# Performance work log

Hardware: AMD Instinct MI355X
Metric: run time of the kernel (lower is better)

Reference implementation:

```python
import jax, jax.numpy as jnp
import numpy as np

S_GRID = 7
B_BOX = 2
N_CLS = 20
N_CH = B_BOX * 5 + N_CLS  # 30
LAMBDA_OBJ = 5.0
LAMBDA_NOOBJ = 0.5
CI = np.array([4, 9])
BI = np.array([0, 1, 2, 3, 5, 6, 7, 8])


def setup_inputs() -> dict:
    key = jax.random.key(0)
    k1, k2 = jax.random.split(key)
    batch = 512
    P = jax.random.uniform(k1, (batch, S_GRID, S_GRID, N_CH), dtype=jnp.float32)
    T = jax.random.uniform(k2, (batch, S_GRID, S_GRID, N_CH), dtype=jnp.float32)
    # deterministic object mask: 1/8 of cells are 'object' cells (channel 4 == 1 exactly)
    cell_idx = jnp.arange(batch * S_GRID * S_GRID).reshape(batch, S_GRID, S_GRID)
    obj_mask = (cell_idx % 8 == 0).astype(jnp.float32)
    T = T.at[..., 4].set(obj_mask)
    return {"P": P, "T": T}


def _norm2dnorm(b, S):
    # (cx, cy, w, h) -> (x1, y1, x2, y2) with cx,cy divided by S
    xy = b[:, :2] / S
    wh = b[:, 2:]
    return jnp.concatenate([xy - 0.5 * wh, xy + 0.5 * wh], axis=-1)


def _iou_mat(b1, b2):
    # b1: (N,4), b2: (M,4) -> (N,M) IoU
    lt = jnp.maximum(b1[:, None, :2], b2[None, :, :2])
    rb = jnp.minimum(b1[:, None, 2:], b2[None, :, 2:])
    wh = jnp.clip(rb - lt, 0.0)
    inter = wh[..., 0] * wh[..., 1]
    a1 = (b1[:, 2] - b1[:, 0]) * (b1[:, 3] - b1[:, 1])
    a2 = (b2[:, 2] - b2[:, 0]) * (b2[:, 3] - b2[:, 1])
    return inter / (a1[:, None] + a2[None, :] - inter)


def reference(P, T):
    batch = P.shape[0]
    Pf = P.reshape(-1, N_CH)
    Tf = T.reshape(-1, N_CH)
    # masks computed on concrete data (static counts by construction)
    obj = np.asarray(Tf[:, 4] == 1.0)
    coord_idx = jnp.asarray(np.nonzero(obj)[0])
    noobj_idx = jnp.asarray(np.nonzero(~obj)[0])

    coordP = Pf[coord_idx]
    coordT = Tf[coord_idx]
    noobjP = Pf[noobj_idx]
    noobjT = Tf[noobj_idx]

    ClassP = coordP[:, B_BOX * 5:]
    ClassT = coordT[:, B_BOX * 5:]
    NoObjP = noobjP[:, CI].reshape(-1)
    NoObjT = noobjT[:, CI].reshape(-1)
    ConfP = coordP[:, CI].reshape(-1)          # (2*Ncoord,)
    BBoxP = coordP[:, BI].reshape(-1, 4)       # (2*Ncoord, 4)
    BBoxT = coordT[:, BI].reshape(-1, 4)

    # original torch code does this under no_grad -> stop_gradient
    BP = jax.lax.stop_gradient(_norm2dnorm(BBoxP, float(S_GRID)))
    BT = jax.lax.stop_gradient(_norm2dnorm(BBoxT, float(S_GRID)))
    M = _iou_mat(BP, BT)                       # (NSize, NSize)
    iou = jax.lax.stop_gradient(jnp.max(M, axis=0))
    idx = jnp.argmax(M, axis=0)                # best pred row per target column

    BPg = BP[idx]
    BTg = BT[idx]
    ConfPg = ConfP[idx]

    lossXY = jnp.sum((BPg[:, :2] - BTg[:, :2]) ** 2)
    lossWH = jnp.sum((jnp.sqrt(BPg[:, 2:]) - jnp.sqrt(BTg[:, 2:])) ** 2)
    lossObj = jnp.sum((ConfPg - iou) ** 2)
    lossNObj = jnp.sum((NoObjP - NoObjT) ** 2)
    lossClass = jnp.sum((ClassP - ClassT) ** 2)

    return (LAMBDA_OBJ * (lossXY + lossWH) + LAMBDA_NOOBJ * lossNObj + (lossObj + lossClass)) / batch
```

## Files before the change

kernel.cpp:

```cpp
#include <hip/hip_runtime.h>
#include <stdint.h>

#define S_GRID 7
#define N_CH 30
#define MAXB 8192
#define NTILE 32
#define NCHUNK 8
#define JG 8


__global__ void k_prep(const float* __restrict__ P, const float* __restrict__ T, int ncell,
                       float4* __restrict__ BP, float4* __restrict__ BT,
                       float* __restrict__ ConfP, float* __restrict__ AreaP,
                       float* __restrict__ pcls, float* __restrict__ pnobj,
                       float* __restrict__ acc, int* __restrict__ finalCtr,
                       int* __restrict__ hdr) {
    int b = blockIdx.x, tid = threadIdx.x;
    int lane = tid & 63, wid = tid >> 6;
    int cell = b * 256 + tid;
    const float* p = P + (size_t)cell * N_CH;
    const float* t = T + (size_t)cell * N_CH;
    bool obj = (cell < ncell) && (t[4] == 1.0f);

    if (b == 0) {
        if (tid < 4)  acc[tid] = 0.0f;
        if (tid == 4) *finalCtr = 0;
    }

    int pre = 0;
    int limit = b * 256;
    for (int c = tid; c < limit; c += 256)
        pre += (T[(size_t)c * N_CH + 4] == 1.0f) ? 1 : 0;
    #pragma unroll
    for (int o = 32; o; o >>= 1) pre += __shfl_down(pre, o);

    unsigned long long bm = __ballot(obj);

    float cls = 0.f, nob = 0.f;
    if (cell < ncell) {
        if (obj) {
            #pragma unroll
            for (int k = 10; k < 30; k++) { float d = p[k] - t[k]; cls += d * d; }
        } else {
            float d0 = p[4] - t[4], d1 = p[9] - t[9];
            nob = d0 * d0 + d1 * d1;
        }
    }
    #pragma unroll
    for (int o = 32; o; o >>= 1) { cls += __shfl_down(cls, o); nob += __shfl_down(nob, o); }

    __shared__ int   shPre[4], shCnt[4], shOfs[4];
    __shared__ float shC[4], shN[4];
    if (lane == 0) {
        shPre[wid] = pre; shCnt[wid] = __popcll(bm);
        shC[wid] = cls;   shN[wid] = nob;
    }
    __syncthreads();
    if (tid == 0) {
        int base = shPre[0] + shPre[1] + shPre[2] + shPre[3];
        int s = 0;
        #pragma unroll
        for (int w = 0; w < 4; w++) { shOfs[w] = base + s; s += shCnt[w]; }
        pcls[b]  = shC[0] + shC[1] + shC[2] + shC[3];
        pnobj[b] = shN[0] + shN[1] + shN[2] + shN[3];
        if (b == gridDim.x - 1) hdr[0] = 2 * (base + s);
    }
    __syncthreads();

    if (obj) {
        int rank = shOfs[wid] + __popcll(bm & ((1ull << lane) - 1ull));
        #pragma unroll
        for (int bb = 0; bb < 2; ++bb) {
            int m = 2 * rank + bb;
            if (m < MAXB) {
                int o5 = bb * 5;
                float cx = p[o5 + 0] / (float)S_GRID, cy = p[o5 + 1] / (float)S_GRID;
                float w = p[o5 + 2], h = p[o5 + 3];
                float4 bp = make_float4(cx - 0.5f * w, cy - 0.5f * h, cx + 0.5f * w, cy + 0.5f * h);
                BP[m] = bp;
                AreaP[m] = (bp.z - bp.x) * (bp.w - bp.y);
                ConfP[m] = p[4 + o5];
                cx = t[o5 + 0] / (float)S_GRID; cy = t[o5 + 1] / (float)S_GRID;
                w = t[o5 + 2]; h = t[o5 + 3];
                BT[m] = make_float4(cx - 0.5f * w, cy - 0.5f * h, cx + 0.5f * w, cy + 0.5f * h);
            }
        }
    }
}

__global__ void k_match(const float4* __restrict__ BP, const float4* __restrict__ BT,
                        const float* __restrict__ AreaP,
                        const int* __restrict__ hdr,
                        unsigned long long* __restrict__ pkeys) {
    int nb = hdr[0]; if (nb > MAXB) nb = MAXB;
    int lane = threadIdx.x & 63, wid = threadIdx.x >> 6;
    int wgrp = blockIdx.x * 4 + wid;
    int j0 = wgrp * JG;
    int c = blockIdx.y;
    int chunkLen = (nb + NCHUNK - 1) / NCHUNK;
    int i0 = c * chunkLen;
    int i1 = min(nb, i0 + chunkLen);
    if (j0 >= nb || i0 >= i1) return;

    float4 tb[JG]; float ta[JG];
    #pragma unroll
    for (int jj = 0; jj < JG; ++jj) {
        float4 t = BT[min(j0 + jj, nb - 1)];
        tb[jj] = t;
        ta[jj] = (t.z - t.x) * (t.w - t.y);
    }
    float bestN[JG], bestD[JG]; int bidx[JG];
    #pragma unroll
    for (int jj = 0; jj < JG; ++jj) { bestN[jj] = -1.f; bestD[jj] = 1.f; bidx[jj] = 0; }

    for (int ib = i0; ib < i1; ib += 64) {
        int i = ib + lane;
        bool v = i < i1;
        int ic = v ? i : i1 - 1;
        float4 pb = BP[ic];
        float a1 = AreaP[ic];
        #pragma unroll
        for (int jj = 0; jj < JG; ++jj) {
            float lx = fmaxf(pb.x, tb[jj].x), ly = fmaxf(pb.y, tb[jj].y);
            float rx = fminf(pb.z, tb[jj].z), ry = fminf(pb.w, tb[jj].w);
            float wx = fmaxf(rx - lx, 0.f), wy = fmaxf(ry - ly, 0.f);
            float inter = wx * wy;
            float u = (a1 + ta[jj]) - inter;
            bool win = v && (inter * bestD[jj] > bestN[jj] * u);
            bestN[jj] = win ? inter : bestN[jj];
            bestD[jj] = win ? u : bestD[jj];
            bidx[jj]  = win ? i : bidx[jj];
        }
    }

    #pragma unroll
    for (int jj = 0; jj < JG; ++jj) {
        unsigned long long key = 0;
        if (bestN[jj] >= 0.f) {
            float r;
            asm("v_rcp_f32 %0, %1" : "=v"(r) : "v"(bestD[jj]));
            float best = bestN[jj] * r;
            key = ((unsigned long long)__float_as_uint(best) << 32) |
                  (unsigned long long)(0xFFFFFFFFu - (unsigned)bidx[jj]);
        }
        #pragma unroll
        for (int o = 32; o; o >>= 1) {
            unsigned lo = (unsigned)key, hi = (unsigned)(key >> 32);
            unsigned lo2 = (unsigned)__shfl_down((int)lo, o);
            unsigned hi2 = (unsigned)__shfl_down((int)hi, o);
            unsigned long long other = ((unsigned long long)hi2 << 32) | lo2;
            if (other > key) key = other;
        }
        if (lane == 0 && j0 + jj < nb)
            pkeys[(size_t)c * MAXB + (j0 + jj)] = key;
    }
}

__global__ void k_gather(const float4* __restrict__ BP, const float4* __restrict__ BT,
                         const float* __restrict__ ConfP,
                         const int* __restrict__ hdr,
                         const unsigned long long* __restrict__ pkeys,
                         const float* __restrict__ pcls, const float* __restrict__ pnobj, int nblk,
                         float* __restrict__ acc, int* __restrict__ finalCtr,
                         float* __restrict__ out, float inv_batch) {
    int nb = hdr[0]; if (nb > MAXB) nb = MAXB;
    int tid = threadIdx.x;
    int j = blockIdx.x * 256 + tid;
    float sxywh = 0.f, sobj = 0.f;
    if (j < nb) {
        int chunkLen = (nb + NCHUNK - 1) / NCHUNK;
        unsigned long long key = 0;
        #pragma unroll
        for (int c = 0; c < NCHUNK; ++c) {
            if (c * chunkLen >= nb) break;
            unsigned long long k2 = pkeys[(size_t)c * MAXB + j];
            if (k2 > key) key = k2;
        }
        float iou = __uint_as_float((unsigned)(key >> 32));
        unsigned idx = 0xFFFFFFFFu - (unsigned)(key & 0xFFFFFFFFull);
        float4 bp = BP[idx], bt = BT[idx];
        float cp = ConfP[idx];
        float dx = bp.x - bt.x, dy = bp.y - bt.y;
        float dw = sqrtf(bp.z) - sqrtf(bt.z);
        float dh = sqrtf(bp.w) - sqrtf(bt.w);
        sxywh = dx * dx + dy * dy + dw * dw + dh * dh;
        float dob = cp - iou;
        sobj = dob * dob;
    }
    float exC = 0.f, exN = 0.f;
    if (blockIdx.x == 0 && tid < nblk) { exC = pcls[tid]; exN = pnobj[tid]; }

    #pragma unroll
    for (int o = 32; o; o >>= 1) {
        sxywh += __shfl_down(sxywh, o); sobj += __shfl_down(sobj, o);
        exC   += __shfl_down(exC, o);   exN  += __shfl_down(exN, o);
    }
    if ((tid & 63) == 0) {
        if (sxywh != 0.f) atomicAdd(&acc[0], sxywh);
        if (sobj != 0.f)  atomicAdd(&acc[1], sobj);
        if (exN != 0.f)   atomicAdd(&acc[2], exN);
        if (exC != 0.f)   atomicAdd(&acc[3], exC);
    }
    __syncthreads();
    if (tid == 0) {
        int old = __hip_atomic_fetch_add(finalCtr, 1, __ATOMIC_ACQ_REL, __HIP_MEMORY_SCOPE_AGENT);
        if (old == NTILE - 1) {
            float a0 = __hip_atomic_load(&acc[0], __ATOMIC_RELAXED, __HIP_MEMORY_SCOPE_AGENT);
            float a1 = __hip_atomic_load(&acc[1], __ATOMIC_RELAXED, __HIP_MEMORY_SCOPE_AGENT);
            float a2 = __hip_atomic_load(&acc[2], __ATOMIC_RELAXED, __HIP_MEMORY_SCOPE_AGENT);
            float a3 = __hip_atomic_load(&acc[3], __ATOMIC_RELAXED, __HIP_MEMORY_SCOPE_AGENT);
            out[0] = (5.0f * a0 + 0.5f * a2 + a1 + a3) * inv_batch;
        }
    }
}

extern "C" void kernel_launch(void* const* d_in, const int* in_sizes, int n_in,
                              void* d_out, int out_size, void* d_ws, size_t ws_size,
                              hipStream_t stream) {
    const float* P = (const float*)d_in[0];
    const float* T = (const float*)d_in[1];
    int ncell = in_sizes[0] / N_CH;
    int batch = ncell / (S_GRID * S_GRID);

    char* ws = (char*)d_ws;
    float* acc      = (float*)ws;
    int*   finalCtr = (int*)(ws + 16);
    int*   hdr      = (int*)(ws + 20);
    float* pcls     = (float*)(ws + 64);
    float* pnobj    = (float*)(ws + 576);
    float4* BP    = (float4*)(ws + 4096);
    float4* BT    = (float4*)(ws + 135168);
    float*  ConfP = (float*)(ws + 266240);
    float*  AreaP = (float*)(ws + 299008);
    unsigned long long* pkeys = (unsigned long long*)(ws + 331776);

    int nblk = (ncell + 255) / 256;
    k_prep  <<<nblk, 256, 0, stream>>>(P, T, ncell, BP, BT, ConfP, AreaP,
                                       pcls, pnobj, acc, finalCtr, hdr);
    dim3 g3(MAXB / (4 * JG), NCHUNK);
    k_match <<<g3, 256, 0, stream>>>(BP, BT, AreaP, hdr, pkeys);
    k_gather<<<NTILE, 256, 0, stream>>>(BP, BT, ConfP, hdr, pkeys, pcls, pnobj, nblk,
                                        acc, finalCtr, (float*)d_out, 1.0f / (float)batch);
}
```

Before: 62.09 us.

## Replace per-block prefix scan with atomic compaction and atomicMax key merge

Each k_prep block used to recount object cells in all earlier blocks to find its output offset, which costs quadratic strided reads of T. Each wavefront now reserves its slot with one atomicAdd on a global counter. k_match merges best-IoU keys straight into a single array with 64-bit atomicMax, so k_final no longer has to reduce per-chunk partial keys, and the match chunk count doubles to 16. Class and no-object sums go directly to global atomics. The cost is one extra tiny init kernel, atomic contention, and an order of compacted boxes that varies from run to run, so argmax tie-breaking and the float summation order can differ between runs.

```diff
diff --git a/kernel.cpp b/kernel.cpp
--- a/kernel.cpp
+++ b/kernel.cpp
@@ -5,36 +5,36 @@
 #define N_CH 30
 #define MAXB 8192
 #define NTILE 32
-#define NCHUNK 8
+#define NCHUNK 16
 #define JG 8
 
 
+__global__ void k_init(float* __restrict__ acc, int* __restrict__ ctr, int* __restrict__ finalCtr) {
+    if (threadIdx.x < 4)  acc[threadIdx.x] = 0.0f;
+    if (threadIdx.x == 4) *ctr = 0;
+    if (threadIdx.x == 5) *finalCtr = 0;
+}
+
 __global__ void k_prep(const float* __restrict__ P, const float* __restrict__ T, int ncell,
+                       int* __restrict__ ctr,
                        float4* __restrict__ BP, float4* __restrict__ BT,
                        float* __restrict__ ConfP, float* __restrict__ AreaP,
-                       float* __restrict__ pcls, float* __restrict__ pnobj,
-                       float* __restrict__ acc, int* __restrict__ finalCtr,
-                       int* __restrict__ hdr) {
-    int b = blockIdx.x, tid = threadIdx.x;
-    int lane = tid & 63, wid = tid >> 6;
-    int cell = b * 256 + tid;
+                       float* __restrict__ acc,
+                       unsigned long long* __restrict__ maxkey) {
+    int gid = blockIdx.x * 256 + threadIdx.x;
+    if (gid < MAXB) maxkey[gid] = 0ull;
+
+    int cell = gid;
     const float* p = P + (size_t)cell * N_CH;
     const float* t = T + (size_t)cell * N_CH;
     bool obj = (cell < ncell) && (t[4] == 1.0f);
 
-    if (b == 0) {
-        if (tid < 4)  acc[tid] = 0.0f;
-        if (tid == 4) *finalCtr = 0;
-    }
-
-    int pre = 0;
-    int limit = b * 256;
-    for (int c = tid; c < limit; c += 256)
-        pre += (T[(size_t)c * N_CH + 4] == 1.0f) ? 1 : 0;
-    #pragma unroll
-    for (int o = 32; o; o >>= 1) pre += __shfl_down(pre, o);
-
+    int lane = threadIdx.x & 63;
     unsigned long long bm = __ballot(obj);
+    int wcnt = __popcll(bm);
+    int base = 0;
+    if (lane == 0 && wcnt) base = atomicAdd(ctr, wcnt);
+    base = __shfl(base, 0);
 
     float cls = 0.f, nob = 0.f;
     if (cell < ncell) {
@@ -48,27 +48,13 @@
     }
     #pragma unroll
     for (int o = 32; o; o >>= 1) { cls += __shfl_down(cls, o); nob += __shfl_down(nob, o); }
-
-    __shared__ int   shPre[4], shCnt[4], shOfs[4];
-    __shared__ float shC[4], shN[4];
     if (lane == 0) {
-        shPre[wid] = pre; shCnt[wid] = __popcll(bm);
-        shC[wid] = cls;   shN[wid] = nob;
-    }
-    __syncthreads();
-    if (tid == 0) {
-        int base = shPre[0] + shPre[1] + shPre[2] + shPre[3];
-        int s = 0;
-        #pragma unroll
-        for (int w = 0; w < 4; w++) { shOfs[w] = base + s; s += shCnt[w]; }
-        pcls[b]  = shC[0] + shC[1] + shC[2] + shC[3];
-        pnobj[b] = shN[0] + shN[1] + shN[2] + shN[3];
-        if (b == gridDim.x - 1) hdr[0] = 2 * (base + s);
-    }
-    __syncthreads();
+        if (cls != 0.f) atomicAdd(&acc[3], cls);
+        if (nob != 0.f) atomicAdd(&acc[2], nob);
+    }
 
     if (obj) {
-        int rank = shOfs[wid] + __popcll(bm & ((1ull << lane) - 1ull));
+        int rank = base + __popcll(bm & ((1ull << lane) - 1ull));
         #pragma unroll
         for (int bb = 0; bb < 2; ++bb) {
             int m = 2 * rank + bb;
@@ -90,9 +76,9 @@
 
 __global__ void k_match(const float4* __restrict__ BP, const float4* __restrict__ BT,
                         const float* __restrict__ AreaP,
-                        const int* __restrict__ hdr,
-                        unsigned long long* __restrict__ pkeys) {
-    int nb = hdr[0]; if (nb > MAXB) nb = MAXB;
+                        const int* __restrict__ ctr,
+                        unsigned long long* __restrict__ maxkey) {
+    int nb = 2 * (*ctr); if (nb > MAXB) nb = MAXB;
     int lane = threadIdx.x & 63, wid = threadIdx.x >> 6;
     int wgrp = blockIdx.x * 4 + wid;
     int j0 = wgrp * JG;
@@ -152,30 +138,22 @@
             if (other > key) key = other;
         }
         if (lane == 0 && j0 + jj < nb)
-            pkeys[(size_t)c * MAXB + (j0 + jj)] = key;
-    }
-}
-
-__global__ void k_gather(const float4* __restrict__ BP, const float4* __restrict__ BT,
-                         const float* __restrict__ ConfP,
-                         const int* __restrict__ hdr,
-                         const unsigned long long* __restrict__ pkeys,
-                         const float* __restrict__ pcls, const float* __restrict__ pnobj, int nblk,
-                         float* __restrict__ acc, int* __restrict__ finalCtr,
-                         float* __restrict__ out, float inv_batch) {
-    int nb = hdr[0]; if (nb > MAXB) nb = MAXB;
+            atomicMax(&maxkey[j0 + jj], key);
+    }
+}
+
+__global__ void k_final(const float4* __restrict__ BP, const float4* __restrict__ BT,
+                        const float* __restrict__ ConfP,
+                        const int* __restrict__ ctr,
+                        const unsigned long long* __restrict__ maxkey,
+                        float* __restrict__ acc, int* __restrict__ finalCtr,
+                        float* __restrict__ out, float inv_batch) {
+    int nb = 2 * (*ctr); if (nb > MAXB) nb = MAXB;
     int tid = threadIdx.x;
     int j = blockIdx.x * 256 + tid;
     float sxywh = 0.f, sobj = 0.f;
     if (j < nb) {
-        int chunkLen = (nb + NCHUNK - 1) / NCHUNK;
-        unsigned long long key = 0;
-        #pragma unroll
-        for (int c = 0; c < NCHUNK; ++c) {
-            if (c * chunkLen >= nb) break;
-            unsigned long long k2 = pkeys[(size_t)c * MAXB + j];
-            if (k2 > key) key = k2;
-        }
+        unsigned long long key = maxkey[j];
         float iou = __uint_as_float((unsigned)(key >> 32));
         unsigned idx = 0xFFFFFFFFu - (unsigned)(key & 0xFFFFFFFFull);
         float4 bp = BP[idx], bt = BT[idx];
@@ -187,19 +165,11 @@
         float dob = cp - iou;
         sobj = dob * dob;
     }
-    float exC = 0.f, exN = 0.f;
-    if (blockIdx.x == 0 && tid < nblk) { exC = pcls[tid]; exN = pnobj[tid]; }
-
-    #pragma unroll
-    for (int o = 32; o; o >>= 1) {
-        sxywh += __shfl_down(sxywh, o); sobj += __shfl_down(sobj, o);
-        exC   += __shfl_down(exC, o);   exN  += __shfl_down(exN, o);
-    }
+    #pragma unroll
+    for (int o = 32; o; o >>= 1) { sxywh += __shfl_down(sxywh, o); sobj += __shfl_down(sobj, o); }
     if ((tid & 63) == 0) {
         if (sxywh != 0.f) atomicAdd(&acc[0], sxywh);
         if (sobj != 0.f)  atomicAdd(&acc[1], sobj);
-        if (exN != 0.f)   atomicAdd(&acc[2], exN);
-        if (exC != 0.f)   atomicAdd(&acc[3], exC);
     }
     __syncthreads();
     if (tid == 0) {
@@ -224,21 +194,19 @@
 
     char* ws = (char*)d_ws;
     float* acc      = (float*)ws;
-    int*   finalCtr = (int*)(ws + 16);
-    int*   hdr      = (int*)(ws + 20);
-    float* pcls     = (float*)(ws + 64);
-    float* pnobj    = (float*)(ws + 576);
-    float4* BP    = (float4*)(ws + 4096);
-    float4* BT    = (float4*)(ws + 135168);
-    float*  ConfP = (float*)(ws + 266240);
-    float*  AreaP = (float*)(ws + 299008);
-    unsigned long long* pkeys = (unsigned long long*)(ws + 331776);
+    int*   ctr      = (int*)(ws + 16);
+    int*   finalCtr = (int*)(ws + 20);
+    unsigned long long* maxkey = (unsigned long long*)(ws + 1024);
+    float4* BP    = (float4*)(ws + 66560);
+    float4* BT    = (float4*)(ws + 197632);
+    float*  ConfP = (float*)(ws + 328704);
+    float*  AreaP = (float*)(ws + 361472);
 
     int nblk = (ncell + 255) / 256;
-    k_prep  <<<nblk, 256, 0, stream>>>(P, T, ncell, BP, BT, ConfP, AreaP,
-                                       pcls, pnobj, acc, finalCtr, hdr);
+    k_init <<<1, 64, 0, stream>>>(acc, ctr, finalCtr);
+    k_prep <<<nblk, 256, 0, stream>>>(P, T, ncell, ctr, BP, BT, ConfP, AreaP, acc, maxkey);
     dim3 g3(MAXB / (4 * JG), NCHUNK);
-    k_match <<<g3, 256, 0, stream>>>(BP, BT, AreaP, hdr, pkeys);
-    k_gather<<<NTILE, 256, 0, stream>>>(BP, BT, ConfP, hdr, pkeys, pcls, pnobj, nblk,
-                                        acc, finalCtr, (float*)d_out, 1.0f / (float)batch);
-}
+    k_match<<<g3, 256, 0, stream>>>(BP, BT, AreaP, ctr, maxkey);
+    k_final<<<NTILE, 256, 0, stream>>>(BP, BT, ConfP, ctr, maxkey, acc, finalCtr,
+                                       (float*)d_out, 1.0f / (float)batch);
+}
```

Result: slower. 68.66 us (+10.6%).
